# Optimization experiments

Hardware: AMD Instinct MI355X
Metric: run time of the kernel (lower is better)

## Reference

```python
import jax, jax.numpy as jnp
import numpy as np

HEAD = 16
EMD = 1024
QK = 64
V = 64
B, SQ, SKV = 4, 2048, 2048


def setup_inputs() -> dict:
    key = jax.random.key(0)
    ks = jax.random.split(key, 10)
    s = 0.02
    return {
        "x_q": jax.random.normal(ks[0], (B, SQ, EMD), dtype=jnp.float32),
        "x_k_v": jax.random.normal(ks[1], (B, SKV, EMD), dtype=jnp.float32),
        "mask_pad": jax.random.randint(ks[2], (B, SQ, SKV), 0, 2) > 0,
        # torch nn.Linear weights: [out_features, in_features]
        "Wq_w": jax.random.normal(ks[3], (QK * HEAD, EMD), dtype=jnp.float32) * s,
        "Wq_b": jnp.zeros((QK * HEAD,), dtype=jnp.float32),
        "Wk_w": jax.random.normal(ks[4], (QK * HEAD, EMD), dtype=jnp.float32) * s,
        "Wk_b": jnp.zeros((QK * HEAD,), dtype=jnp.float32),
        "Wv_w": jax.random.normal(ks[5], (V * HEAD, EMD), dtype=jnp.float32) * s,
        "Wv_b": jnp.zeros((V * HEAD,), dtype=jnp.float32),
    }


def reference(x_q, x_k_v, mask_pad, Wq_w, Wq_b, Wk_w, Wk_b, Wv_w, Wv_b):
    b, sq, _ = x_q.shape
    skv = x_k_v.shape[1]
    q = x_q @ Wq_w.T + Wq_b            # [B, SQ, H*QK]
    k = x_k_v @ Wk_w.T + Wk_b          # [B, SKV, H*QK]
    v = x_k_v @ Wv_w.T + Wv_b          # [B, SKV, H*V]
    q = q.reshape(b, sq, HEAD, QK).transpose(0, 2, 1, 3)   # [B, H, SQ, QK]
    k = k.reshape(b, skv, HEAD, QK).transpose(0, 2, 1, 3)  # [B, H, SKV, QK]
    v = v.reshape(b, skv, HEAD, V).transpose(0, 2, 1, 3)   # [B, H, SKV, V]
    scale = 1.0 / jnp.sqrt(jnp.float32(QK))
    atten = jnp.einsum('bhqd,bhkd->bhqk', q, k) * scale    # [B, H, SQ, SKV]
    atten = jnp.where(mask_pad[:, None, :, :], jnp.float32(-1e9), atten)
    atten = jax.nn.softmax(atten, axis=-1)
    z = jnp.einsum('bhqk,bhkv->bhqv', atten, v)            # [B, H, SQ, V]
    z = z.transpose(0, 2, 1, 3).reshape(b, sq, HEAD * V)   # [B, SQ, H*V]
    return z
```

## Files before the change

### kernel.cpp

```cpp
#include <hip/hip_runtime.h>
#include <stdint.h>

#define HEADS 16
#define EMDIM 1024
#define DHEAD 64
#define BATCH 4
#define SEQQ 2048
#define SEQK 2048
#define NT (SEQK / 64)
#define QSCALE 0.18033688011112042f

typedef __attribute__((ext_vector_type(8))) short bf16x8;
typedef __attribute__((ext_vector_type(4))) float f32x4;
typedef __attribute__((ext_vector_type(4))) unsigned int u32x4;

typedef __attribute__((address_space(3))) void lds_void;
typedef const __attribute__((address_space(1))) void gbl_void;
#define GL_LDS16(g, l) __builtin_amdgcn_global_load_lds((gbl_void*)(g), (lds_void*)(l), 16, 0, 0)
#define MFMA16(a, b, c) __builtin_amdgcn_mfma_f32_16x16x32_bf16(a, b, c, 0, 0, 0)

__device__ __forceinline__ unsigned short f2bf(float f) {
    unsigned int u = __builtin_bit_cast(unsigned int, f);
    u += 0x7fffu + ((u >> 16) & 1u);
    return (unsigned short)(u >> 16);
}

__device__ __forceinline__ void exp2x4(float& a, float& b, float& c, float& d) {
    asm("v_exp_f32 %0, %0\n\t"
        "v_exp_f32 %1, %1\n\t"
        "v_exp_f32 %2, %2\n\t"
        "v_exp_f32 %3, %3\n\t"
        "s_nop 0"
        : "+v"(a), "+v"(b), "+v"(c), "+v"(d));
}

__device__ __forceinline__ unsigned int cvtpk_bf16(float lo, float hi) {
    unsigned int r;
    asm("v_cvt_pk_bf16_f32 %0, %1, %2" : "=v"(r) : "v"(lo), "v"(hi));
    return r;
}

__global__ __launch_bounds__(256) void prep_all(const float* __restrict__ xq,
                                                const float* __restrict__ xkv,
                                                const float* __restrict__ wq,
                                                const float* __restrict__ wk,
                                                const float* __restrict__ wv,
                                                unsigned short* __restrict__ oxq,
                                                unsigned short* __restrict__ oxkv,
                                                unsigned short* __restrict__ owq,
                                                unsigned short* __restrict__ owk,
                                                unsigned short* __restrict__ owv,
                                                const void* __restrict__ mask,
                                                unsigned long long* __restrict__ packed) {
    const int NX = (BATCH * SEQQ * EMDIM) / 4;
    const int NW = (EMDIM * EMDIM) / 4;
    const int total = 2 * NX + 3 * NW;
    for (int i = blockIdx.x * 256 + threadIdx.x; i < total; i += gridDim.x * 256) {
        const float* src;
        unsigned short* dst;
        int j = i;
        if (j < NX) { src = xq; dst = oxq; }
        else if ((j -= NX) < NX) { src = xkv; dst = oxkv; }
        else if ((j -= NX) < NW) { src = wq; dst = owq; }
        else if ((j -= NW) < NW) { src = wk; dst = owk; }
        else { j -= NW; src = wv; dst = owv; }
        float4 v = reinterpret_cast<const float4*>(src)[j];
        ushort4 o;
        o.x = f2bf(v.x); o.y = f2bf(v.y); o.z = f2bf(v.z); o.w = f2bf(v.w);
        reinterpret_cast<ushort4*>(dst)[j] = o;
    }
    const int* mi = (const int*)mask;
    const uint8_t* mu = (const uint8_t*)mask;
    const int lane = threadIdx.x & 63;
    const bool u8src = __any(((unsigned)mi[lane]) > 1u);
    const size_t N = (size_t)BATCH * SEQQ * SEQK;
    const size_t stride = (size_t)gridDim.x * blockDim.x;
    for (size_t idx = (size_t)blockIdx.x * blockDim.x + threadIdx.x; idx < N; idx += stride) {
        const int v = u8src ? (int)mu[idx] : mi[idx];
        const unsigned long long bb = __ballot(v != 0);
        if (lane == 0) packed[idx >> 6] = bb;
    }
}

__global__ __launch_bounds__(256) void gemm_qkv(
    const unsigned short* __restrict__ xq, const unsigned short* __restrict__ xkv,
    const unsigned short* __restrict__ Wqm, const unsigned short* __restrict__ Wkm,
    const unsigned short* __restrict__ Wvm,
    const float* __restrict__ bq, const float* __restrict__ bk, const float* __restrict__ bv,
    unsigned short* __restrict__ Qo, unsigned short* __restrict__ Ko,
    unsigned short* __restrict__ Vo) {
    __shared__ __align__(16) unsigned short Alds[128 * 64];
    __shared__ __align__(16) unsigned short Blds[128 * 64];

    const int rawid = blockIdx.y * gridDim.x + blockIdx.x;
    const int xcd = rawid & 7;
    const int slot = rawid >> 3;
    const int nb = xcd * 3 + slot % 3;
    const int mt = slot / 3;
    const int m0 = mt * 128;
    const int which = nb >> 3;
    const unsigned short* A = (which == 0) ? xq : xkv;
    const unsigned short* W = (which == 0) ? Wqm : (which == 1) ? Wkm : Wvm;
    const float* bias = (which == 0) ? bq : (which == 1) ? bk : bv;
    const int n0 = (nb & 7) * 128;

    const int tid = threadIdx.x;
    const int lane = tid & 63;
    const int wid = tid >> 6;
    const int wm = wid >> 1, wn = wid & 1;
    const int lq = lane & 15, lh = lane >> 4;

    f32x4 acc[4][4] = {};

    const int srow = tid >> 3;
    const int scol = (tid & 7) * 8;

    for (int kt = 0; kt < 16; ++kt) {
        const int kb = kt * 64;
#pragma unroll
        for (int i = 0; i < 4; ++i) {
            const int row = i * 32 + srow;
            GL_LDS16(&A[(size_t)(m0 + row) * EMDIM + kb + scol], &Alds[row * 64 + scol]);
            GL_LDS16(&W[(size_t)(n0 + row) * EMDIM + kb + scol], &Blds[row * 64 + scol]);
        }
        __syncthreads();
#pragma unroll
        for (int ks = 0; ks < 2; ++ks) {
            bf16x8 af[4], bfr[4];
#pragma unroll
            for (int mf = 0; mf < 4; ++mf)
                af[mf] = *(const bf16x8*)&Alds[(wm * 64 + mf * 16 + lq) * 64 + ks * 32 + lh * 8];
#pragma unroll
            for (int nf = 0; nf < 4; ++nf)
                bfr[nf] = *(const bf16x8*)&Blds[(wn * 64 + nf * 16 + lq) * 64 + ks * 32 + lh * 8];
#pragma unroll
            for (int mf = 0; mf < 4; ++mf)
#pragma unroll
                for (int nf = 0; nf < 4; ++nf)
                    acc[mf][nf] = MFMA16(af[mf], bfr[nf], acc[mf][nf]);
        }
        __syncthreads();
    }

#pragma unroll
    for (int nf = 0; nf < 4; ++nf) {
        const int n = n0 + wn * 64 + nf * 16 + lq;
        const float bvv = bias[n];
        const int h = n >> 6, d = n & 63;
#pragma unroll
        for (int mf = 0; mf < 4; ++mf) {
            const int mbase = m0 + wm * 64 + mf * 16 + lh * 4;
            const int b = mbase >> 11;
            const int s = mbase & 2047;
            if (which == 2) {
                ushort4 pk;
                pk.x = f2bf(acc[mf][nf][0] + bvv);
                pk.y = f2bf(acc[mf][nf][1] + bvv);
                pk.z = f2bf(acc[mf][nf][2] + bvv);
                pk.w = f2bf(acc[mf][nf][3] + bvv);
                *(ushort4*)&Vo[(((size_t)(b * HEADS + h) * DHEAD) + d) * SEQK + s] = pk;
            } else {
                const float sc = (which == 0) ? QSCALE : 1.0f;
                unsigned short* o = (which == 0) ? Qo : Ko;
#pragma unroll
                for (int r = 0; r < 4; ++r) {
                    float v = (acc[mf][nf][r] + bvv) * sc;
                    o[(((size_t)(b * HEADS + h) * SEQQ) + (s + r)) * DHEAD + d] = f2bf(v);
                }
            }
        }
    }
}

__global__ __launch_bounds__(256, 3) void attn_fused(const unsigned short* __restrict__ Q,
                                                     const unsigned short* __restrict__ K,
                                                     const unsigned short* __restrict__ VT,
                                                     const unsigned long long* __restrict__ mpk,
                                                     float* __restrict__ out) {
    const int tid = threadIdx.x;
    const int lane = tid & 63;
    const int wid = tid >> 6;
    const int lq = lane & 15, lh = lane >> 4;
    const int bh = blockIdx.x;
    const int b = bh >> 4, h = bh & 15;
    const int qbase = blockIdx.y * 128 + wid * 32;

    __shared__ __align__(16) unsigned short Kl[2][64 * 64];
    __shared__ __align__(16) unsigned short Vl[2][64 * 64];

    const unsigned short* Kbh = K + (size_t)bh * SEQK * DHEAD;
    const unsigned short* Vbh = VT + (size_t)bh * DHEAD * SEQK;

    bf16x8 bq[2][2];
    const unsigned long long* mrow[2];
#pragma unroll
    for (int sub = 0; sub < 2; ++sub) {
        const int q = qbase + sub * 16 + lq;
        const unsigned short* qrow = Q + ((size_t)bh * SEQQ + q) * DHEAD;
        bq[sub][0] = *(const bf16x8*)&qrow[lh * 8];
        bq[sub][1] = *(const bf16x8*)&qrow[32 + lh * 8];
        mrow[sub] = mpk + ((size_t)b * SEQQ + q) * NT;
    }

    f32x4 acc[4][2] = {};
    f32x4 accl[2] = {};

    const bf16x8 vone = {16256, 16256, 16256, 16256, 16256, 16256, 16256, 16256};

    const int srow8 = lane >> 3;
    const int sg = (lane & 7) ^ srow8;
    const int g7 = lq & 7;

    auto stage = [&](int s, int t) {
        const int k0 = t * 64;
#pragma unroll
        for (int i = 0; i < 2; ++i) {
            const int cc = wid * 2 + i;
            const int r = cc * 8 + srow8;
            GL_LDS16(Kbh + (size_t)(k0 + r) * DHEAD + sg * 8, &Kl[s][cc * 512]);
            GL_LDS16(Vbh + (size_t)r * SEQK + k0 + sg * 8, &Vl[s][cc * 512]);
        }
    };

    unsigned long long mwc[2], mwn[2];
#pragma unroll
    for (int sub = 0; sub < 2; ++sub) mwc[sub] = mrow[sub][0];

    stage(0, 0);
    __syncthreads();
    int cur = 0;

    for (int t = 0; t < NT; ++t) {
        if (t < NT - 1) {
            stage(cur ^ 1, t + 1);
#pragma unroll
            for (int sub = 0; sub < 2; ++sub) mwn[sub] = mrow[sub][t + 1];
        }

        uint2 w[2][4];
#pragma unroll
        for (int kb = 0; kb < 4; ++kb) {
            const unsigned short* kr = &Kl[cur][(kb * 16 + lq) * 64];
            const bf16x8 a0 = *(const bf16x8*)&kr[((0 + lh) ^ g7) * 8];
            const bf16x8 a1 = *(const bf16x8*)&kr[((4 + lh) ^ g7) * 8];
#pragma unroll
            for (int sub = 0; sub < 2; ++sub) {
                f32x4 z = {};
                z = MFMA16(a0, bq[sub][0], z);
                z = MFMA16(a1, bq[sub][1], z);
                const unsigned int ml = (unsigned int)(mwc[sub] >> (kb * 16 + lh * 4));
                float p0 = (ml & 1u) ? -1e9f : z[0];
                float p1 = (ml & 2u) ? -1e9f : z[1];
                float p2 = (ml & 4u) ? -1e9f : z[2];
                float p3 = (ml & 8u) ? -1e9f : z[3];
                exp2x4(p0, p1, p2, p3);
                w[sub][kb].x = cvtpk_bf16(p0, p1);
                w[sub][kb].y = cvtpk_bf16(p2, p3);
            }
        }

        bf16x8 pf[2][2];
#pragma unroll
        for (int sub = 0; sub < 2; ++sub) {
#pragma unroll
            for (int ks = 0; ks < 2; ++ks) {
                unsigned int s0 = w[sub][2 * ks].x, s2 = w[sub][2 * ks + 1].x;
                unsigned int s1 = w[sub][2 * ks].y, s3 = w[sub][2 * ks + 1].y;
                asm("v_permlane32_swap_b32 %0, %1" : "+v"(s0), "+v"(s2));
                asm("v_permlane32_swap_b32 %0, %1" : "+v"(s1), "+v"(s3));
                asm("v_permlane16_swap_b32 %0, %1" : "+v"(s0), "+v"(s2));
                asm("v_permlane16_swap_b32 %0, %1" : "+v"(s1), "+v"(s3));
                u32x4 fd = {s0, s1, s2, s3};
                pf[sub][ks] = __builtin_bit_cast(bf16x8, fd);
            }
        }

        __builtin_amdgcn_s_setprio(1);
#pragma unroll
        for (int sub = 0; sub < 2; ++sub) {
            accl[sub] = MFMA16(vone, pf[sub][0], accl[sub]);
            accl[sub] = MFMA16(vone, pf[sub][1], accl[sub]);
        }
#pragma unroll
        for (int vb = 0; vb < 4; ++vb) {
            const unsigned short* vr = &Vl[cur][(vb * 16 + lq) * 64];
            const bf16x8 av0 = *(const bf16x8*)&vr[((0 + lh) ^ g7) * 8];
            const bf16x8 av1 = *(const bf16x8*)&vr[((4 + lh) ^ g7) * 8];
#pragma unroll
            for (int sub = 0; sub < 2; ++sub) {
                acc[vb][sub] = MFMA16(av0, pf[sub][0], acc[vb][sub]);
                acc[vb][sub] = MFMA16(av1, pf[sub][1], acc[vb][sub]);
            }
        }
        __builtin_amdgcn_s_setprio(0);

        __syncthreads();
        cur ^= 1;
#pragma unroll
        for (int sub = 0; sub < 2; ++sub) mwc[sub] = mwn[sub];
    }

#pragma unroll
    for (int sub = 0; sub < 2; ++sub) {
        const float rl = 1.f / accl[sub][0];
        const int q = qbase + sub * 16 + lq;
        float* orow = out + ((size_t)b * SEQQ + q) * (HEADS * DHEAD) + h * DHEAD;
#pragma unroll
        for (int vb = 0; vb < 4; ++vb) {
            float4 o4;
            o4.x = acc[vb][sub][0] * rl;
            o4.y = acc[vb][sub][1] * rl;
            o4.z = acc[vb][sub][2] * rl;
            o4.w = acc[vb][sub][3] * rl;
            *(float4*)&orow[vb * 16 + lh * 4] = o4;
        }
    }
}

extern "C" void kernel_launch(void* const* d_in, const int* in_sizes, int n_in,
                              void* d_out, int out_size, void* d_ws, size_t ws_size,
                              hipStream_t stream) {
    const float* x_q  = (const float*)d_in[0];
    const float* x_kv = (const float*)d_in[1];
    const void*  mask = (const void*)d_in[2];
    const float* Wq_w = (const float*)d_in[3];
    const float* Wq_b = (const float*)d_in[4];
    const float* Wk_w = (const float*)d_in[5];
    const float* Wk_b = (const float*)d_in[6];
    const float* Wv_w = (const float*)d_in[7];
    const float* Wv_b = (const float*)d_in[8];
    float* out = (float*)d_out;

    char* ws = (char*)d_ws;
    const size_t SZ_QKV = (size_t)BATCH * HEADS * SEQQ * DHEAD * sizeof(unsigned short);
    const size_t SZ_X   = (size_t)BATCH * SEQQ * EMDIM * sizeof(unsigned short);
    const size_t SZ_W   = (size_t)EMDIM * EMDIM * sizeof(unsigned short);
    unsigned short* Qb  = (unsigned short*)(ws);
    unsigned short* Kb  = (unsigned short*)(ws + SZ_QKV);
    unsigned short* VTb = (unsigned short*)(ws + 2 * SZ_QKV);
    unsigned short* xqb = (unsigned short*)(ws + 3 * SZ_QKV);
    unsigned short* xkb = (unsigned short*)(ws + 3 * SZ_QKV + SZ_X);
    unsigned short* Wqb = (unsigned short*)(ws + 3 * SZ_QKV + 2 * SZ_X);
    unsigned short* Wkb = (unsigned short*)(ws + 3 * SZ_QKV + 2 * SZ_X + SZ_W);
    unsigned short* Wvb = (unsigned short*)(ws + 3 * SZ_QKV + 2 * SZ_X + 2 * SZ_W);
    unsigned long long* mpk = (unsigned long long*)(ws + 3 * SZ_QKV + 2 * SZ_X + 3 * SZ_W);

    prep_all<<<2048, 256, 0, stream>>>(x_q, x_kv, Wq_w, Wk_w, Wv_w, xqb, xkb, Wqb, Wkb, Wvb,
                                       mask, mpk);

    dim3 ggrid(24, BATCH * SEQQ / 128);
    gemm_qkv<<<ggrid, 256, 0, stream>>>(xqb, xkb, Wqb, Wkb, Wvb, Wq_b, Wk_b, Wv_b, Qb, Kb, VTb);

    dim3 agrid(BATCH * HEADS, SEQQ / 128);
    attn_fused<<<agrid, 256, 0, stream>>>(Qb, Kb, VTb, mpk, out);
}
```

Measured before the change: 216.6 us.

## Double-buffer LDS tiles in QKV projection GEMM to overlap loads with MFMA

The QKV GEMM now keeps two LDS buffers for each of A and B. The next K-tile's global-to-LDS loads are issued before computing the current tile, with a partial vmcnt wait so loads overlap the MFMA work. It also raises wave priority around the MFMA block. This doubles LDS use to 64KB per block, which may reduce occupancy, and it relies on hand-placed waitcnt and barrier ordering being correct.

```diff
diff --git a/kernel.cpp b/kernel.cpp
--- a/kernel.cpp
+++ b/kernel.cpp
@@ -89,8 +89,8 @@
     const float* __restrict__ bq, const float* __restrict__ bk, const float* __restrict__ bv,
     unsigned short* __restrict__ Qo, unsigned short* __restrict__ Ko,
     unsigned short* __restrict__ Vo) {
-    __shared__ __align__(16) unsigned short Alds[128 * 64];
-    __shared__ __align__(16) unsigned short Blds[128 * 64];
+    __shared__ __align__(16) unsigned short Alds[2][128 * 64];
+    __shared__ __align__(16) unsigned short Blds[2][128 * 64];
 
     const int rawid = blockIdx.y * gridDim.x + blockIdx.x;
     const int xcd = rawid & 7;
@@ -115,31 +115,46 @@
     const int srow = tid >> 3;
     const int scol = (tid & 7) * 8;
 
-    for (int kt = 0; kt < 16; ++kt) {
+    auto stage = [&](int s, int kt) {
         const int kb = kt * 64;
 #pragma unroll
         for (int i = 0; i < 4; ++i) {
             const int row = i * 32 + srow;
-            GL_LDS16(&A[(size_t)(m0 + row) * EMDIM + kb + scol], &Alds[row * 64 + scol]);
-            GL_LDS16(&W[(size_t)(n0 + row) * EMDIM + kb + scol], &Blds[row * 64 + scol]);
-        }
-        __syncthreads();
+            GL_LDS16(&A[(size_t)(m0 + row) * EMDIM + kb + scol], &Alds[s][row * 64 + scol]);
+            GL_LDS16(&W[(size_t)(n0 + row) * EMDIM + kb + scol], &Blds[s][row * 64 + scol]);
+        }
+    };
+
+    stage(0, 0);
+    int cur = 0;
+    for (int kt = 0; kt < 16; ++kt) {
+        if (kt < 15) {
+            stage(cur ^ 1, kt + 1);
+            asm volatile("s_waitcnt vmcnt(8)" ::: "memory");
+        } else {
+            asm volatile("s_waitcnt vmcnt(0)" ::: "memory");
+        }
+        __builtin_amdgcn_s_barrier();
 #pragma unroll
         for (int ks = 0; ks < 2; ++ks) {
             bf16x8 af[4], bfr[4];
 #pragma unroll
             for (int mf = 0; mf < 4; ++mf)
-                af[mf] = *(const bf16x8*)&Alds[(wm * 64 + mf * 16 + lq) * 64 + ks * 32 + lh * 8];
+                af[mf] = *(const bf16x8*)&Alds[cur][(wm * 64 + mf * 16 + lq) * 64 + ks * 32 + lh * 8];
 #pragma unroll
             for (int nf = 0; nf < 4; ++nf)
-                bfr[nf] = *(const bf16x8*)&Blds[(wn * 64 + nf * 16 + lq) * 64 + ks * 32 + lh * 8];
+                bfr[nf] = *(const bf16x8*)&Blds[cur][(wn * 64 + nf * 16 + lq) * 64 + ks * 32 + lh * 8];
+            __builtin_amdgcn_s_setprio(1);
 #pragma unroll
             for (int mf = 0; mf < 4; ++mf)
 #pragma unroll
                 for (int nf = 0; nf < 4; ++nf)
                     acc[mf][nf] = MFMA16(af[mf], bfr[nf], acc[mf][nf]);
-        }
-        __syncthreads();
+            __builtin_amdgcn_s_setprio(0);
+        }
+        asm volatile("s_waitcnt lgkmcnt(0)" ::: "memory");
+        __builtin_amdgcn_s_barrier();
+        cur ^= 1;
     }
 
 #pragma unroll
```

After: 212.5 us. No clear change (-1.9%).
